# Performance work log

Measured on AMD Instinct MI355X. Metric: run time of the kernel, lower is better.

## Reference

```python
import jax, jax.numpy as jnp
import numpy as np

N_NODES = 10000
N_EDGES = 640000
N_GRAPHS = 100
D_FEAT = 128
D_HID = 512


def setup_inputs() -> dict:
    key = jax.random.key(0)
    ks = jax.random.split(key, 6)
    nodes = jax.random.normal(ks[0], (N_NODES, D_FEAT), jnp.float32)
    edges = jax.random.uniform(ks[1], (N_EDGES, 1), jnp.float32)  # per-edge regularization weight
    senders = jax.random.randint(ks[2], (N_EDGES,), 0, N_NODES, jnp.int32)
    receivers = jax.random.randint(ks[3], (N_EDGES,), 0, N_NODES, jnp.int32)
    n_node = jnp.full((N_GRAPHS,), N_NODES // N_GRAPHS, jnp.int32)
    n_edge = jnp.full((N_GRAPHS,), N_EDGES // N_GRAPHS, jnp.int32)
    W1 = jax.random.normal(ks[4], (D_FEAT, D_HID), jnp.float32) / np.float32(np.sqrt(D_FEAT))
    b1 = jnp.zeros((D_HID,), jnp.float32)
    W2 = jax.random.normal(ks[5], (D_HID, D_FEAT), jnp.float32) / np.float32(np.sqrt(D_HID))
    b2 = jnp.zeros((D_FEAT,), jnp.float32)
    return dict(nodes=nodes, edges=edges, senders=senders, receivers=receivers,
                n_node=n_node, n_edge=n_edge, W1=W1, b1=b1, W2=W2, b2=b2)


def reference(nodes, edges, senders, receivers, n_node, n_edge, W1, b1, W2, b2):
    G = n_node.shape[0]
    E = edges.shape[0]
    # graph id for each edge (EdgesToGlobalsAggregator segment ids)
    edge_gid = jnp.repeat(jnp.arange(G, dtype=jnp.int32), n_edge, total_repeat_length=E)
    w = edges[:, 0]  # [E] edge weights
    # example_weights = unsorted_segment_sum of edge features per graph
    example_weights = jax.ops.segment_sum(w, edge_gid, num_segments=G)  # [G]
    # GraphIndependent node model: MLP applied per node
    h = jax.nn.relu(nodes @ W1 + b1) @ W2 + b2  # [N, D]
    # EdgeRelationNetwork edge block: gather sender/receiver features, weighted L2 distance
    src = jnp.take(h, senders, axis=0)     # [E, D]
    dst = jnp.take(h, receivers, axis=0)   # [E, D]
    edge_out = w * jnp.sum(jnp.square(src - dst), axis=-1)  # [E]
    # aggregate edges -> globals (unsorted_segment_sum)
    globals_agg = jax.ops.segment_sum(edge_out, edge_gid, num_segments=G)  # [G]
    # graph loss: mean(divide_no_nan(globals, example_weights))
    graph_loss = jnp.mean(jnp.where(example_weights != 0.0,
                                    globals_agg / jnp.where(example_weights != 0.0, example_weights, 1.0),
                                    0.0))
    # NodeGraphModel output: node features at last node of each graph
    node_ids = jnp.cumsum(n_node) - 1  # [G]
    node_out = jnp.take(h, node_ids, axis=0)  # [G, D]
    return node_out, graph_loss
```

## Files before the change

### kernel.cpp

```cpp
#include <hip/hip_runtime.h>

#define D_F 128
#define D_H 512
#define SHS 520

typedef short v8s __attribute__((ext_vector_type(8)));
typedef float v4f __attribute__((ext_vector_type(4)));
typedef _Float16 v2h __attribute__((ext_vector_type(2)));

__device__ inline unsigned short f2bf(float f) {
    unsigned u = __float_as_uint(f);
    unsigned r = (u + 0x7fffu + ((u >> 16) & 1u)) >> 16;
    return (unsigned short)r;
}
__device__ inline v2h bch(unsigned x) { return __builtin_bit_cast(v2h, x); }

__global__ __launch_bounds__(256) void prep_kernel(
    const float* __restrict__ W1, const float* __restrict__ W2,
    const int* __restrict__ n_node, const int* __restrict__ n_edge,
    unsigned short* __restrict__ W1T, unsigned short* __restrict__ W2T,
    int* __restrict__ ec, int* __restrict__ nid,
    float* __restrict__ ew, float* __restrict__ ga, int G, int E)
{
    if (blockIdx.x == 0) {
        __shared__ int sne[512];
        __shared__ int snn[512];
        const int t = threadIdx.x;
        for (int g = t; g < G; g += 256) { sne[g] = n_edge[g]; snn[g] = n_node[g]; }
        __syncthreads();
        for (int g = t; g < G; g += 256) {
            int se = 0, sn = 0;
            for (int k = 0; k < g; ++k)  se += sne[k];
            for (int k = 0; k <= g; ++k) sn += snn[k];
            ec[g]  = se;
            nid[g] = sn - 1;
            ew[g] = 0.f;
            ga[g] = 0.f;
            if (g == G - 1) {
                int tot = se + sne[g];
                ec[G] = tot > E ? tot : E;
            }
        }
    }
    int i = blockIdx.x * 256 + threadIdx.x;
    if (i < D_F * D_H) {
        int n = i >> 7, k = i & (D_F - 1);
        W1T[i] = f2bf(W1[k * D_H + n]);
        int n2 = i >> 9, k2 = i & (D_H - 1);
        W2T[i] = f2bf(W2[k2 * D_F + n2]);
    }
}

__global__ __launch_bounds__(512) void mlp_mfma_kernel(
    const float* __restrict__ nodes,
    const unsigned short* __restrict__ W1T, const float* __restrict__ b1,
    const unsigned short* __restrict__ W2T, const float* __restrict__ b2,
    _Float16* __restrict__ hh, int N)
{
    __shared__ unsigned short sH[16 * SHS];

    const int t    = threadIdx.x;
    const int wave = t >> 6;
    const int lane = t & 63;
    const int li   = lane & 15;
    const int quad = lane >> 4;
    const int row0 = blockIdx.x * 16;

    v8s a1[4];
    {
        int r = min(row0 + li, N - 1);
        const float* xp = nodes + (size_t)r * D_F + quad * 8;
        #pragma unroll
        for (int ks = 0; ks < 4; ++ks) {
            float4 f0 = *(const float4*)(xp + ks * 32);
            float4 f1 = *(const float4*)(xp + ks * 32 + 4);
            v8s v;
            v[0] = (short)f2bf(f0.x); v[1] = (short)f2bf(f0.y);
            v[2] = (short)f2bf(f0.z); v[3] = (short)f2bf(f0.w);
            v[4] = (short)f2bf(f1.x); v[5] = (short)f2bf(f1.y);
            v[6] = (short)f2bf(f1.z); v[7] = (short)f2bf(f1.w);
            a1[ks] = v;
        }
    }

    #pragma unroll 2
    for (int jj = 0; jj < 4; ++jj) {
        const int n0 = (wave * 4 + jj) * 16;
        const unsigned short* wp = W1T + (size_t)(n0 + li) * D_F + quad * 8;
        v4f acc = {0.f, 0.f, 0.f, 0.f};
        #pragma unroll
        for (int ks = 0; ks < 4; ++ks) {
            v8s b = *(const v8s*)(wp + ks * 32);
            acc = __builtin_amdgcn_mfma_f32_16x16x32_bf16(a1[ks], b, acc, 0, 0, 0);
        }
        float bias = b1[n0 + li];
        #pragma unroll
        for (int r = 0; r < 4; ++r) {
            float hv = fmaxf(acc[r] + bias, 0.f);
            int m = quad * 4 + r;
            sH[m * SHS + n0 + li] = f2bf(hv);
        }
    }
    __syncthreads();

    v8s aH[16];
    #pragma unroll
    for (int ks = 0; ks < 16; ++ks)
        aH[ks] = *(const v8s*)(sH + li * SHS + ks * 32 + quad * 8);

    {
        const int n0 = wave * 16;
        const unsigned short* wp = W2T + (size_t)(n0 + li) * D_H + quad * 8;
        v4f acc = {0.f, 0.f, 0.f, 0.f};
        #pragma unroll
        for (int kc = 0; kc < 2; ++kc) {
            v8s bb[8];
            #pragma unroll
            for (int u = 0; u < 8; ++u)
                bb[u] = *(const v8s*)(wp + (kc * 8 + u) * 32);
            #pragma unroll
            for (int u = 0; u < 8; ++u)
                acc = __builtin_amdgcn_mfma_f32_16x16x32_bf16(aH[kc * 8 + u], bb[u], acc, 0, 0, 0);
        }
        float bias = b2[n0 + li];
        #pragma unroll
        for (int r = 0; r < 4; ++r) {
            int grow = row0 + quad * 4 + r;
            if (grow < N)
                hh[(size_t)grow * D_F + n0 + li] = (_Float16)(acc[r] + bias);
        }
    }
}

__global__ __launch_bounds__(512) void edge_kernel(
    const _Float16* __restrict__ hh, const float* __restrict__ wedge,
    const int* __restrict__ senders, const int* __restrict__ receivers,
    const int* __restrict__ ec,
    float* __restrict__ ew, float* __restrict__ ga,
    int E, int G)
{
    __shared__ int   sec[513];
    __shared__ float sga[512];
    __shared__ float sew[512];
    const int t = threadIdx.x;
    for (int i = t; i <= G; i += 512) sec[i] = ec[i];
    for (int i = t; i < G;  i += 512) { sga[i] = 0.f; sew[i] = 0.f; }
    __syncthreads();

    const unsigned* __restrict__ h32 = (const unsigned*)hh;
    const int lane = t & 63;
    const int tb   = (blockIdx.x * 8 + (t >> 6)) << 6;

    if (tb < E) {
        const int tbu = __builtin_amdgcn_readfirstlane(tb);
        const int nt  = min(64, E - tbu);

        int gid;
        { int lo = 0, hi = G - 1;
          while (lo < hi) { int m = (lo + hi + 1) >> 1; if (sec[m] <= tbu) lo = m; else hi = m - 1; }
          gid = lo; }

        const int*   __restrict__ sp = senders   + tbu;
        const int*   __restrict__ rp = receivers + tbu;
        const float* __restrict__ wp = wedge     + tbu;

        if (nt == 64 && tbu + 64 <= sec[gid + 1]) {
            float accE = 0.f, accW = 0.f;
            #pragma unroll 1
            for (int i = 0; i < 64; i += 32) {
                unsigned a[32], b[32];
                #pragma unroll
                for (int u = 0; u < 32; ++u) {
                    int s = sp[i + u];
                    int r = rp[i + u];
                    a[u] = h32[(unsigned)((s << 6) | lane)];
                    b[u] = h32[(unsigned)((r << 6) | lane)];
                }
                #pragma unroll
                for (int u = 0; u < 32; ++u) {
                    float w = wp[i + u];
                    v2h d  = bch(a[u]) - bch(b[u]);
                    float tt = __builtin_amdgcn_fdot2(d, d, 0.f, false);
                    accE = fmaf(w, tt, accE);
                    accW += w;
                }
            }
            float rE = accE;
            #pragma unroll
            for (int m = 32; m > 0; m >>= 1) rE += __shfl_xor(rE, m);
            if (lane == 0) {
                atomicAdd(&sga[gid], rE);
                atomicAdd(&sew[gid], accW);
            }
        } else {
            float accE = 0.f, accW = 0.f;
            for (int i = 0; i < nt; ++i) {
                int e = tbu + i;
                while (e >= sec[gid + 1]) {
                    float rE = accE;
                    #pragma unroll
                    for (int m = 32; m > 0; m >>= 1) rE += __shfl_xor(rE, m);
                    if (lane == 0 && (rE != 0.f || accW != 0.f)) {
                        atomicAdd(&sga[gid], rE);
                        atomicAdd(&sew[gid], accW);
                    }
                    accE = 0.f; accW = 0.f;
                    ++gid;
                }
                int   s = sp[i];
                int   r = rp[i];
                float w = wp[i];
                unsigned a = h32[(unsigned)((s << 6) | lane)];
                unsigned b = h32[(unsigned)((r << 6) | lane)];
                v2h d = bch(a) - bch(b);
                float tt = __builtin_amdgcn_fdot2(d, d, 0.f, false);
                accE = fmaf(w, tt, accE);
                accW += w;
            }
            float rE = accE;
            #pragma unroll
            for (int m = 32; m > 0; m >>= 1) rE += __shfl_xor(rE, m);
            if (lane == 0 && (rE != 0.f || accW != 0.f)) {
                atomicAdd(&sga[gid], rE);
                atomicAdd(&sew[gid], accW);
            }
        }
    }

    __syncthreads();
    for (int g = t; g < G; g += 512) {
        float vg = sga[g], vw = sew[g];
        if (vg != 0.f || vw != 0.f) {
            atomicAdd(&ga[g], vg);
            atomicAdd(&ew[g], vw);
        }
    }
}

__global__ __launch_bounds__(128) void finalize_kernel(
    const _Float16* __restrict__ hh, const int* __restrict__ nid,
    const float* __restrict__ ew, const float* __restrict__ ga,
    float* __restrict__ out, int G)
{
    const int g = blockIdx.x;
    const int t = threadIdx.x;
    if (g < G) {
        int src = nid[g];
        out[(size_t)g * D_F + t] = (float)hh[(size_t)src * D_F + t];
    } else {
        float p = 0.f;
        for (int i = t; i < G; i += 128) {
            float w = ew[i];
            p += (w != 0.f) ? ga[i] / w : 0.f;
        }
        #pragma unroll
        for (int m = 32; m > 0; m >>= 1) p += __shfl_xor(p, m);
        __shared__ float sp[2];
        if ((t & 63) == 0) sp[t >> 6] = p;
        __syncthreads();
        if (t == 0) out[(size_t)G * D_F] = (sp[0] + sp[1]) / (float)G;
    }
}

extern "C" void kernel_launch(void* const* d_in, const int* in_sizes, int n_in,
                              void* d_out, int out_size, void* d_ws, size_t ws_size,
                              hipStream_t stream) {
    const float* nodes     = (const float*)d_in[0];
    const float* edges     = (const float*)d_in[1];
    const int*   senders   = (const int*)d_in[2];
    const int*   receivers = (const int*)d_in[3];
    const int*   n_node    = (const int*)d_in[4];
    const int*   n_edge    = (const int*)d_in[5];
    const float* W1        = (const float*)d_in[6];
    const float* b1        = (const float*)d_in[7];
    const float* W2        = (const float*)d_in[8];
    const float* b2        = (const float*)d_in[9];

    const int N = in_sizes[0] / D_F;
    const int E = in_sizes[1];
    const int G = in_sizes[4];

    float* out = (float*)d_out;

    _Float16*       hh  = (_Float16*)d_ws;
    unsigned short* W1T = (unsigned short*)(hh + (size_t)N * D_F);
    unsigned short* W2T = W1T + (size_t)D_F * D_H;
    int*            ec  = (int*)(W2T + (size_t)D_F * D_H);
    int*            nid = ec + (G + 1);
    float*          ew  = (float*)(nid + G);
    float*          ga  = ew + G;

    prep_kernel<<<(D_F * D_H + 255) / 256, 256, 0, stream>>>(
        W1, W2, n_node, n_edge, W1T, W2T, ec, nid, ew, ga, G, E);

    const int nblk = (N + 15) / 16;
    mlp_mfma_kernel<<<nblk, 512, 0, stream>>>(nodes, W1T, b1, W2T, b2, hh, N);

    const int ntiles = (E + 63) / 64;
    const int nblkE  = (ntiles + 7) / 8;
    edge_kernel<<<nblkE, 512, 0, stream>>>(hh, edges, senders, receivers, ec,
                                           ew, ga, E, G);

    finalize_kernel<<<G + 1, 128, 0, stream>>>(hh, nid, ew, ga, out, G);
}
```

Before: 131.1 us.

## Gather 16-byte row chunks per lane in edge kernel; double MLP rows per block

The edge kernel now has each group of 16 lanes load a full 256-byte fp16 row with 16-byte loads, so one wave handles 4 edges per load step instead of 1 edge per 64 4-byte loads. The goal is fewer, wider gather instructions and more memory-level parallelism. The edge-weight sum is now reduced across lanes and scaled by 1/16 to undo the replicated counting. Separately, the MLP kernel processes 32 rows per block with two accumulators, so each W1/W2 fragment load is reused twice, at the cost of more LDS and registers.

```diff
diff --git a/kernel.cpp b/kernel.cpp
--- a/kernel.cpp
+++ b/kernel.cpp
@@ -57,18 +57,19 @@
     const unsigned short* __restrict__ W2T, const float* __restrict__ b2,
     _Float16* __restrict__ hh, int N)
 {
-    __shared__ unsigned short sH[16 * SHS];
+    __shared__ unsigned short sH[32 * SHS];
 
     const int t    = threadIdx.x;
     const int wave = t >> 6;
     const int lane = t & 63;
     const int li   = lane & 15;
     const int quad = lane >> 4;
-    const int row0 = blockIdx.x * 16;
-
-    v8s a1[4];
-    {
-        int r = min(row0 + li, N - 1);
+    const int row0 = blockIdx.x * 32;
+
+    v8s a1[2][4];
+    #pragma unroll
+    for (int rg = 0; rg < 2; ++rg) {
+        int r = min(row0 + rg * 16 + li, N - 1);
         const float* xp = nodes + (size_t)r * D_F + quad * 8;
         #pragma unroll
         for (int ks = 0; ks < 4; ++ks) {
@@ -79,7 +80,7 @@
             v[2] = (short)f2bf(f0.z); v[3] = (short)f2bf(f0.w);
             v[4] = (short)f2bf(f1.x); v[5] = (short)f2bf(f1.y);
             v[6] = (short)f2bf(f1.z); v[7] = (short)f2bf(f1.w);
-            a1[ks] = v;
+            a1[rg][ks] = v;
         }
     }
 
@@ -87,47 +88,52 @@
     for (int jj = 0; jj < 4; ++jj) {
         const int n0 = (wave * 4 + jj) * 16;
         const unsigned short* wp = W1T + (size_t)(n0 + li) * D_F + quad * 8;
-        v4f acc = {0.f, 0.f, 0.f, 0.f};
+        v4f acc0 = {0.f, 0.f, 0.f, 0.f};
+        v4f acc1 = {0.f, 0.f, 0.f, 0.f};
         #pragma unroll
         for (int ks = 0; ks < 4; ++ks) {
             v8s b = *(const v8s*)(wp + ks * 32);
-            acc = __builtin_amdgcn_mfma_f32_16x16x32_bf16(a1[ks], b, acc, 0, 0, 0);
+            acc0 = __builtin_amdgcn_mfma_f32_16x16x32_bf16(a1[0][ks], b, acc0, 0, 0, 0);
+            acc1 = __builtin_amdgcn_mfma_f32_16x16x32_bf16(a1[1][ks], b, acc1, 0, 0, 0);
         }
         float bias = b1[n0 + li];
         #pragma unroll
         for (int r = 0; r < 4; ++r) {
-            float hv = fmaxf(acc[r] + bias, 0.f);
             int m = quad * 4 + r;
-            sH[m * SHS + n0 + li] = f2bf(hv);
+            sH[m * SHS + n0 + li]        = f2bf(fmaxf(acc0[r] + bias, 0.f));
+            sH[(16 + m) * SHS + n0 + li] = f2bf(fmaxf(acc1[r] + bias, 0.f));
         }
     }
     __syncthreads();
-
-    v8s aH[16];
-    #pragma unroll
-    for (int ks = 0; ks < 16; ++ks)
-        aH[ks] = *(const v8s*)(sH + li * SHS + ks * 32 + quad * 8);
 
     {
         const int n0 = wave * 16;
         const unsigned short* wp = W2T + (size_t)(n0 + li) * D_H + quad * 8;
-        v4f acc = {0.f, 0.f, 0.f, 0.f};
-        #pragma unroll
-        for (int kc = 0; kc < 2; ++kc) {
-            v8s bb[8];
+        v4f acc0 = {0.f, 0.f, 0.f, 0.f};
+        v4f acc1 = {0.f, 0.f, 0.f, 0.f};
+        #pragma unroll
+        for (int kc = 0; kc < 4; ++kc) {
+            v8s bb[4], aH0[4], aH1[4];
             #pragma unroll
-            for (int u = 0; u < 8; ++u)
-                bb[u] = *(const v8s*)(wp + (kc * 8 + u) * 32);
+            for (int u = 0; u < 4; ++u) {
+                int ks = kc * 4 + u;
+                bb[u]  = *(const v8s*)(wp + ks * 32);
+                aH0[u] = *(const v8s*)(sH + li * SHS + ks * 32 + quad * 8);
+                aH1[u] = *(const v8s*)(sH + (16 + li) * SHS + ks * 32 + quad * 8);
+            }
             #pragma unroll
-            for (int u = 0; u < 8; ++u)
-                acc = __builtin_amdgcn_mfma_f32_16x16x32_bf16(aH[kc * 8 + u], bb[u], acc, 0, 0, 0);
+            for (int u = 0; u < 4; ++u) {
+                acc0 = __builtin_amdgcn_mfma_f32_16x16x32_bf16(aH0[u], bb[u], acc0, 0, 0, 0);
+                acc1 = __builtin_amdgcn_mfma_f32_16x16x32_bf16(aH1[u], bb[u], acc1, 0, 0, 0);
+            }
         }
         float bias = b2[n0 + li];
         #pragma unroll
         for (int r = 0; r < 4; ++r) {
-            int grow = row0 + quad * 4 + r;
-            if (grow < N)
-                hh[(size_t)grow * D_F + n0 + li] = (_Float16)(acc[r] + bias);
+            int g0 = row0 + quad * 4 + r;
+            if (g0 < N) hh[(size_t)g0 * D_F + n0 + li] = (_Float16)(acc0[r] + bias);
+            int g1 = row0 + 16 + quad * 4 + r;
+            if (g1 < N) hh[(size_t)g1 * D_F + n0 + li] = (_Float16)(acc1[r] + bias);
         }
     }
 }
@@ -148,6 +154,7 @@
     __syncthreads();
 
     const unsigned* __restrict__ h32 = (const unsigned*)hh;
+    const uint4*    __restrict__ h16 = (const uint4*)hh;
     const int lane = t & 63;
     const int tb   = (blockIdx.x * 8 + (t >> 6)) << 6;
 
@@ -165,32 +172,55 @@
         const float* __restrict__ wp = wedge     + tbu;
 
         if (nt == 64 && tbu + 64 <= sec[gid + 1]) {
+            const bool q0 = (lane & 16) != 0;
+            const bool q1 = (lane & 32) != 0;
+            const int  c  = lane & 15;
             float accE = 0.f, accW = 0.f;
             #pragma unroll 1
             for (int i = 0; i < 64; i += 32) {
-                unsigned a[32], b[32];
+                uint4 a[8], b[8];
                 #pragma unroll
-                for (int u = 0; u < 32; ++u) {
-                    int s = sp[i + u];
-                    int r = rp[i + u];
-                    a[u] = h32[(unsigned)((s << 6) | lane)];
-                    b[u] = h32[(unsigned)((r << 6) | lane)];
+                for (int u = 0; u < 8; ++u) {
+                    int e = i + u * 4;
+                    int s0 = sp[e], s1 = sp[e + 1], s2 = sp[e + 2], s3 = sp[e + 3];
+                    int r0 = rp[e], r1 = rp[e + 1], r2 = rp[e + 2], r3 = rp[e + 3];
+                    int sA = q0 ? s1 : s0;
+                    int sB = q0 ? s3 : s2;
+                    int s  = q1 ? sB : sA;
+                    int rA = q0 ? r1 : r0;
+                    int rB = q0 ? r3 : r2;
+                    int r  = q1 ? rB : rA;
+                    a[u] = h16[(unsigned)((s << 4) | c)];
+                    b[u] = h16[(unsigned)((r << 4) | c)];
                 }
                 #pragma unroll
-                for (int u = 0; u < 32; ++u) {
-                    float w = wp[i + u];
-                    v2h d  = bch(a[u]) - bch(b[u]);
-                    float tt = __builtin_amdgcn_fdot2(d, d, 0.f, false);
+                for (int u = 0; u < 8; ++u) {
+                    int e = i + u * 4;
+                    float w0 = wp[e], w1 = wp[e + 1], w2 = wp[e + 2], w3 = wp[e + 3];
+                    float wA = q0 ? w1 : w0;
+                    float wB = q0 ? w3 : w2;
+                    float w  = q1 ? wB : wA;
+                    v2h d0 = bch(a[u].x) - bch(b[u].x);
+                    v2h d1 = bch(a[u].y) - bch(b[u].y);
+                    v2h d2 = bch(a[u].z) - bch(b[u].z);
+                    v2h d3 = bch(a[u].w) - bch(b[u].w);
+                    float tt = __builtin_amdgcn_fdot2(d0, d0, 0.f, false);
+                    tt = __builtin_amdgcn_fdot2(d1, d1, tt, false);
+                    tt = __builtin_amdgcn_fdot2(d2, d2, tt, false);
+                    tt = __builtin_amdgcn_fdot2(d3, d3, tt, false);
                     accE = fmaf(w, tt, accE);
                     accW += w;
                 }
             }
-            float rE = accE;
+            float rE = accE, rW = accW;
             #pragma unroll
-            for (int m = 32; m > 0; m >>= 1) rE += __shfl_xor(rE, m);
+            for (int m = 32; m > 0; m >>= 1) {
+                rE += __shfl_xor(rE, m);
+                rW += __shfl_xor(rW, m);
+            }
             if (lane == 0) {
                 atomicAdd(&sga[gid], rE);
-                atomicAdd(&sew[gid], accW);
+                atomicAdd(&sew[gid], rW * 0.0625f);
             }
         } else {
             float accE = 0.f, accW = 0.f;
@@ -293,7 +323,7 @@
     prep_kernel<<<(D_F * D_H + 255) / 256, 256, 0, stream>>>(
         W1, W2, n_node, n_edge, W1T, W2T, ec, nid, ew, ga, G, E);
 
-    const int nblk = (N + 15) / 16;
+    const int nblk = (N + 31) / 32;
     mlp_mfma_kernel<<<nblk, 512, 0, stream>>>(nodes, W1T, b1, W2T, b2, hh, N);
 
     const int ntiles = (E + 63) / 64;
```

Result: no change. 128.6 us (median of 2 runs) (-1.9%).
